# Kernel optimization log

Hardware: AMD Instinct MI355X
Metric: run time of the kernel (lower is better)

## Reference

```python
import jax, jax.numpy as jnp
import numpy as np

B, S, D_MODEL = 2, 2048, 512
KEY_DIM, VALUE_DIM, OUTPUT_DIM, NUM_HEADS = 256, 256, 512, 8


def setup_inputs() -> dict:
    key = jax.random.key(0)
    ks = jax.random.split(key, 12)
    s = 0.02
    return {
        "V": jax.random.normal(ks[0], (B, S, D_MODEL), jnp.float32),
        "Q": jax.random.normal(ks[1], (B, S, D_MODEL), jnp.float32),
        "K": jax.random.normal(ks[2], (B, S, D_MODEL), jnp.float32),
        "mask": jax.random.normal(ks[3], (B, 1, S, S), jnp.float32),
        "Wq": jax.random.normal(ks[4], (D_MODEL, KEY_DIM), jnp.float32) * s,
        "bq": jnp.zeros((KEY_DIM,), jnp.float32),
        "Wk": jax.random.normal(ks[5], (D_MODEL, KEY_DIM), jnp.float32) * s,
        "bk": jnp.zeros((KEY_DIM,), jnp.float32),
        "Wv": jax.random.normal(ks[6], (D_MODEL, VALUE_DIM), jnp.float32) * s,
        "bv": jnp.zeros((VALUE_DIM,), jnp.float32),
        "Wo": jax.random.normal(ks[7], (VALUE_DIM, OUTPUT_DIM), jnp.float32) * s,
        "bo": jnp.zeros((OUTPUT_DIM,), jnp.float32),
    }


def _split_heads(x, num_heads):
    # [B, S, H*d] -> [B, H, S, d]
    b, s, hd = x.shape
    return x.reshape(b, s, num_heads, hd // num_heads).transpose(0, 2, 1, 3)


def reference(V, Q, K, mask, Wq, bq, Wk, bk, Wv, bv, Wo, bo):
    denom = jnp.sqrt(jnp.float32(KEY_DIM))  # NOTE: full key_dim, as in source
    q = _split_heads(Q @ Wq + bq, NUM_HEADS)  # [B,H,S,dk]
    k = _split_heads(K @ Wk + bk, NUM_HEADS)
    scores = jnp.einsum("bhqd,bhkd->bhqk", q, k) / denom
    scores = scores + mask  # soft (additive) mask
    weights = jax.nn.softmax(scores, axis=-1)
    v = _split_heads(V @ Wv + bv, NUM_HEADS)  # [B,H,S,dv]
    ctx = jnp.einsum("bhqk,bhkd->bhqd", weights, v)  # [B,H,S,dv]
    b, h, s, d = ctx.shape
    ctx = ctx.transpose(0, 2, 1, 3).reshape(b, s, h * d)  # merge heads
    return ctx @ Wo + bo
```

## Files before the change

kernel.cpp:

```cpp
#include <hip/hip_runtime.h>

typedef __attribute__((ext_vector_type(8))) short bf16x8;
typedef __attribute__((ext_vector_type(4))) float f32x4;

#define B_  2
#define S_  2048
#define DM  512
#define KD  256
#define HD  32
#define NH  8

__device__ __forceinline__ float bf2f(ushort u) {
    return __uint_as_float(((uint)u) << 16);
}
__device__ __forceinline__ ushort f2bf(float f) {
    uint x = __float_as_uint(f);
    return (ushort)((x + 0x7fffu + ((x >> 16) & 1u)) >> 16);
}
#define MFMA __builtin_amdgcn_mfma_f32_16x16x32_bf16

__global__ void detect_dtype(const ushort* __restrict__ q, int* __restrict__ flag)
{
    int lane = threadIdx.x & 63;
    int cnt = 0;
    for (int i = lane; i < 256; i += 64) {
        int e = (q[i] >> 7) & 0xFF;
        if (e >= 100 && e <= 133) ++cnt;
    }
    #pragma unroll
    for (int off = 32; off; off >>= 1) cnt += __shfl_down(cnt, off, 64);
    if (lane == 0) *flag = (cnt >= 230) ? 1 : 0;
}

__global__ __launch_bounds__(256) void convert_x(
    const void* __restrict__ Q, const void* __restrict__ K, const void* __restrict__ V,
    const int* __restrict__ flag, ushort* __restrict__ Xb)
{
    int isbf = *flag;
    int y = blockIdx.y;
    int tid = blockIdx.x * 256 + threadIdx.x;
    const void* X = (y == 0) ? Q : (y == 1) ? K : V;
    ushort* dst = Xb + (size_t)y * (4096 * 512) + (size_t)tid * 8;
    if (isbf) {
        *(bf16x8*)dst = *((const bf16x8*)X + tid);
    } else {
        const float* s = (const float*)X + (size_t)tid * 8;
        bf16x8 v8;
        #pragma unroll
        for (int j = 0; j < 8; ++j) v8[j] = (short)f2bf(s[j]);
        *(bf16x8*)dst = v8;
    }
}

__global__ __launch_bounds__(256) void transpose_w(
    const void* __restrict__ Wq, const void* __restrict__ Wk, const void* __restrict__ Wv,
    const void* __restrict__ Wo,
    const void* __restrict__ bq, const void* __restrict__ bk,
    const void* __restrict__ bv, const void* __restrict__ bo,
    const int* __restrict__ flag,
    ushort* __restrict__ Wt, ushort* __restrict__ Wot, float* __restrict__ biasf)
{
    int isbf = *flag;
    int bid = blockIdx.x;
    if (bid >= 512) {
        for (int i = threadIdx.x; i < 1280; i += 256) {
            const void* bp; int off;
            if (i < 256)      { bp = bq; off = i; }
            else if (i < 512) { bp = bk; off = i - 256; }
            else if (i < 768) { bp = bv; off = i - 512; }
            else              { bp = bo; off = i - 768; }
            biasf[i] = isbf ? bf2f(((const ushort*)bp)[off]) : ((const float*)bp)[off];
        }
        return;
    }
    const void* W; int R, C; ushort* T;
    int m = bid >> 7, tix = bid & 127;
    if (m < 3) { W = (m == 0) ? Wq : (m == 1) ? Wk : Wv; R = 512; C = 256; T = Wt + m * 131072; }
    else       { W = Wo; R = 256; C = 512; T = Wot; }
    int tilesPerRow = C >> 5;
    int r0 = (tix / tilesPerRow) * 32, c0 = (tix % tilesPerRow) * 32;
    __shared__ float lds[32][33];
    int t = threadIdx.x;
    int rr = t >> 3, cc = (t & 7) * 4;
    if (isbf) {
        const ushort* Ws = (const ushort*)W;
        #pragma unroll
        for (int j = 0; j < 4; ++j) lds[rr][cc + j] = bf2f(Ws[(size_t)(r0 + rr) * C + c0 + cc + j]);
    } else {
        float4 v = *(const float4*)((const float*)W + (size_t)(r0 + rr) * C + c0 + cc);
        lds[rr][cc + 0] = v.x; lds[rr][cc + 1] = v.y; lds[rr][cc + 2] = v.z; lds[rr][cc + 3] = v.w;
    }
    __syncthreads();
    ushort4 o;
    o.x = f2bf(lds[cc + 0][rr]); o.y = f2bf(lds[cc + 1][rr]);
    o.z = f2bf(lds[cc + 2][rr]); o.w = f2bf(lds[cc + 3][rr]);
    *(ushort4*)(T + (size_t)(c0 + rr) * R + r0 + cc) = o;
}

__global__ __launch_bounds__(256) void qkv_gemm(
    const ushort* __restrict__ Xb, const ushort* __restrict__ Wt,
    const float* __restrict__ biasf,
    ushort* __restrict__ qh, ushort* __restrict__ kh, ushort* __restrict__ vh)
{
    int y = blockIdx.y;
    int wave = threadIdx.x >> 6, lane = threadIdx.x & 63;
    int l16 = lane & 15, quad = lane >> 4;
    int m0 = blockIdx.x * 32;
    int n0 = wave * 64;
    const ushort* X = Xb + (size_t)y * (4096 * 512);
    const ushort* W = Wt + (size_t)y * (256 * 512);
    f32x4 acc[2][4] = {};
    for (int ks = 0; ks < 512; ks += 32) {
        bf16x8 a[2], b[4];
        #pragma unroll
        for (int i = 0; i < 2; ++i)
            a[i] = *(const bf16x8*)(X + (size_t)(m0 + 16 * i + l16) * 512 + ks + quad * 8);
        #pragma unroll
        for (int j = 0; j < 4; ++j)
            b[j] = *(const bf16x8*)(W + (size_t)(n0 + 16 * j + l16) * 512 + ks + quad * 8);
        #pragma unroll
        for (int i = 0; i < 2; ++i)
            #pragma unroll
            for (int j = 0; j < 4; ++j)
                acc[i][j] = MFMA(a[i], b[j], acc[i][j], 0, 0, 0);
    }
    ushort* out = (y == 0) ? qh : (y == 1) ? kh : vh;
    #pragma unroll
    for (int i = 0; i < 2; ++i) {
        #pragma unroll
        for (int j = 0; j < 4; ++j) {
            int n = n0 + 16 * j + l16;
            float bs = biasf[y * 256 + n];
            int h = n >> 5, d = n & 31;
            #pragma unroll
            for (int r = 0; r < 4; ++r) {
                int rg = m0 + 16 * i + quad * 4 + r;
                int bb = rg >> 11, ss = rg & 2047;
                out[((((size_t)bb * NH + h) * S_ + ss) << 5) + d] = f2bf(acc[i][j][r] + bs);
            }
        }
    }
}

__global__ __launch_bounds__(256) void transpose_v(
    const ushort* __restrict__ vh, ushort* __restrict__ vT)
{
    __shared__ ushort lds[32][66];
    int bh = blockIdx.x >> 5;
    int s0 = (blockIdx.x & 31) * 64;
    int t = threadIdx.x;
    const ushort* src = vh + ((size_t)bh * S_ + s0) * HD;
    #pragma unroll
    for (int it = 0; it < 8; ++it) {
        int e = it * 256 + t;
        lds[e & 31][e >> 5] = src[e];
    }
    __syncthreads();
    ushort* dst = vT + (size_t)bh * HD * S_ + s0;
    #pragma unroll
    for (int it = 0; it < 8; ++it) {
        int e = it * 256 + t;
        dst[(size_t)(e >> 6) * S_ + (e & 63)] = lds[e >> 6][e & 63];
    }
}

__global__ __launch_bounds__(256) void attn(
    const ushort* __restrict__ qh, const ushort* __restrict__ kh,
    const ushort* __restrict__ vT, const void* __restrict__ maskp,
    const int* __restrict__ flag, float* __restrict__ pO, float* __restrict__ pl)
{
    __shared__ __align__(16) float  ldsM[4][16][68];
    __shared__ __align__(16) ushort ldsP[4][16][72];
    int isbf = *flag;
    int wave = threadIdx.x >> 6, lane = threadIdx.x & 63;
    int l16 = lane & 15, quad = lane >> 4;
    int wid = blockIdx.x * 4 + wave;
    int chunk = wid & 1, qt = (wid >> 1) & 127, bh = wid >> 8;
    int b = bh >> 3;
    int q0 = qt * 16;
    const ushort* qb = qh + (size_t)bh * S_ * HD;
    const ushort* kb = kh + (size_t)bh * S_ * HD;
    const ushort* vb = vT + (size_t)bh * HD * S_;
    const ushort* mbb = (const ushort*)maskp + (size_t)b * S_ * S_;
    const float*  mbf = (const float*)maskp  + (size_t)b * S_ * S_;

    bf16x8 aq = *(const bf16x8*)(qb + (size_t)(q0 + l16) * HD + quad * 8);
    f32x4 O0 = {0, 0, 0, 0}, O1 = {0, 0, 0, 0};
    const f32x4 zero = {0, 0, 0, 0};
    float lsum[4] = {0, 0, 0, 0};

    auto loadT = [&](int k0, float4* M, bf16x8* Kf, bf16x8* Vf) {
        if (isbf) {
            #pragma unroll
            for (int it = 0; it < 4; ++it) {
                ushort4 u = *(const ushort4*)(mbb + (size_t)(q0 + it * 4 + quad) * S_ + k0 + l16 * 4);
                float4 f; f.x = bf2f(u.x); f.y = bf2f(u.y); f.z = bf2f(u.z); f.w = bf2f(u.w);
                M[it] = f;
            }
        } else {
            #pragma unroll
            for (int it = 0; it < 4; ++it)
                M[it] = *(const float4*)(mbf + (size_t)(q0 + it * 4 + quad) * S_ + k0 + l16 * 4);
        }
        #pragma unroll
        for (int c = 0; c < 4; ++c)
            Kf[c] = *(const bf16x8*)(kb + (size_t)(k0 + c * 16 + l16) * HD + quad * 8);
        Vf[0] = *(const bf16x8*)(vb + (size_t)l16 * S_ + k0 + quad * 8);
        Vf[1] = *(const bf16x8*)(vb + (size_t)l16 * S_ + k0 + 32 + quad * 8);
        Vf[2] = *(const bf16x8*)(vb + (size_t)(16 + l16) * S_ + k0 + quad * 8);
        Vf[3] = *(const bf16x8*)(vb + (size_t)(16 + l16) * S_ + k0 + 32 + quad * 8);
    };

    auto tilestep = [&](float4* M, bf16x8* Kf, bf16x8* Vf,
                        int nextk0, float4* Mn, bf16x8* Kn, bf16x8* Vn) {
        #pragma unroll
        for (int it = 0; it < 4; ++it)
            *(float4*)&ldsM[wave][it * 4 + quad][l16 * 4] = M[it];
        if (nextk0 >= 0) loadT(nextk0, Mn, Kn, Vn);
        f32x4 Sc[4];
        #pragma unroll
        for (int c = 0; c < 4; ++c) Sc[c] = MFMA(aq, Kf[c], zero, 0, 0, 0);
        asm volatile("s_waitcnt lgkmcnt(0)" ::: "memory");
        #pragma unroll
        for (int c = 0; c < 4; ++c) {
            #pragma unroll
            for (int r = 0; r < 4; ++r) {
                float mv = ldsM[wave][quad * 4 + r][c * 16 + l16];
                float s = fminf(Sc[c][r] * 0.0625f + mv, 30.0f);
                float p = __expf(s);
                lsum[r] += p;
                ldsP[wave][quad * 4 + r][c * 16 + l16] = f2bf(p);
            }
        }
        asm volatile("s_waitcnt lgkmcnt(0)" ::: "memory");
        bf16x8 aP0 = *(const bf16x8*)&ldsP[wave][l16][quad * 8];
        bf16x8 aP1 = *(const bf16x8*)&ldsP[wave][l16][32 + quad * 8];
        O0 = MFMA(aP0, Vf[0], O0, 0, 0, 0);
        O0 = MFMA(aP1, Vf[1], O0, 0, 0, 0);
        O1 = MFMA(aP0, Vf[2], O1, 0, 0, 0);
        O1 = MFMA(aP1, Vf[3], O1, 0, 0, 0);
    };

    int kbase = chunk * 1024;
    float4 Ma[4], Mb2[4]; bf16x8 Ka[4], Kb2[4], Va[4], Vb2[4];
    loadT(kbase, Ma, Ka, Va);
    for (int t = 0; t < 16; t += 2) {
        tilestep(Ma, Ka, Va, kbase + (t + 1) * 64, Mb2, Kb2, Vb2);
        tilestep(Mb2, Kb2, Vb2, (t + 2 < 16) ? kbase + (t + 2) * 64 : -1, Ma, Ka, Va);
    }

    float* po = pO + (size_t)wid * 512;
    #pragma unroll
    for (int r = 0; r < 4; ++r) {
        int row = quad * 4 + r;
        po[row * 32 + l16]      = O0[r];
        po[row * 32 + 16 + l16] = O1[r];
        float sthis = lsum[r];
        #pragma unroll
        for (int off = 8; off; off >>= 1) sthis += __shfl_xor(sthis, off, 16);
        if (l16 == 0) pl[wid * 16 + row] = sthis;
    }
}

__global__ __launch_bounds__(256) void combine(
    const float* __restrict__ pO, const float* __restrict__ pl, ushort* __restrict__ ctx)
{
    int e = blockIdx.x * 256 + threadIdx.x;
    int d = e & 31;
    int row = (e >> 5) & 2047;
    int bh = e >> 16;
    int qt = row >> 4, r16 = row & 15;
    int wid0 = (bh << 8) | (qt << 1);
    float o = pO[(size_t)wid0 * 512 + r16 * 32 + d] + pO[(size_t)(wid0 + 1) * 512 + r16 * 32 + d];
    float l = pl[wid0 * 16 + r16] + pl[(wid0 + 1) * 16 + r16];
    int b = bh >> 3, h = bh & 7;
    ctx[((size_t)(b * S_ + row)) * KD + h * HD + d] = f2bf(o / l);
}

__global__ __launch_bounds__(256) void out_proj(
    const ushort* __restrict__ ctx, const ushort* __restrict__ Wot,
    const float* __restrict__ biasf, float* __restrict__ out)
{
    int wave = threadIdx.x >> 6, lane = threadIdx.x & 63;
    int l16 = lane & 15, quad = lane >> 4;
    int m0 = (blockIdx.x >> 1) * 32;
    int n0 = (blockIdx.x & 1) * 256 + wave * 64;
    f32x4 acc[2][4] = {};
    for (int ks = 0; ks < 256; ks += 32) {
        bf16x8 a[2], b[4];
        #pragma unroll
        for (int i = 0; i < 2; ++i)
            a[i] = *(const bf16x8*)(ctx + (size_t)(m0 + 16 * i + l16) * 256 + ks + quad * 8);
        #pragma unroll
        for (int j = 0; j < 4; ++j)
            b[j] = *(const bf16x8*)(Wot + (size_t)(n0 + 16 * j + l16) * 256 + ks + quad * 8);
        #pragma unroll
        for (int i = 0; i < 2; ++i)
            #pragma unroll
            for (int j = 0; j < 4; ++j)
                acc[i][j] = MFMA(a[i], b[j], acc[i][j], 0, 0, 0);
    }
    #pragma unroll
    for (int i = 0; i < 2; ++i) {
        #pragma unroll
        for (int j = 0; j < 4; ++j) {
            int n = n0 + 16 * j + l16;
            float bs = biasf[768 + n];
            #pragma unroll
            for (int r = 0; r < 4; ++r) {
                int rg = m0 + 16 * i + quad * 4 + r;
                out[(size_t)rg * DM + n] = acc[i][j][r] + bs;
            }
        }
    }
}

extern "C" void kernel_launch(void* const* d_in, const int* in_sizes, int n_in,
                              void* d_out, int out_size, void* d_ws, size_t ws_size,
                              hipStream_t stream)
{
    const void* V    = d_in[0];
    const void* Q    = d_in[1];
    const void* K    = d_in[2];
    const void* mask = d_in[3];
    const void* Wq = d_in[4];  const void* bq = d_in[5];
    const void* Wk = d_in[6];  const void* bk = d_in[7];
    const void* Wv = d_in[8];  const void* bv = d_in[9];
    const void* Wo = d_in[10]; const void* bo = d_in[11];
    float* out = (float*)d_out;

    char* ws = (char*)d_ws;
    int*    flagp = (int*)ws;
    float*  biasf = (float*)(ws + 128);
    ushort* qh  = (ushort*)(ws + 8192);
    ushort* kh  = qh  + 1048576;
    ushort* vh_ = kh  + 1048576;
    ushort* vT  = vh_ + 1048576;
    ushort* ctx = vT  + 1048576;
    ushort* Wt  = ctx + 1048576;
    ushort* Wot = Wt  + 393216;
    ushort* Xb  = Wot + 131072;
    float* pO = (float*)Xb;
    float* pl = pO + 4096 * 512;

    detect_dtype<<<1, 64, 0, stream>>>((const ushort*)Q, flagp);
    convert_x<<<dim3(1024, 3), 256, 0, stream>>>(Q, K, V, flagp, Xb);
    transpose_w<<<513, 256, 0, stream>>>(Wq, Wk, Wv, Wo, bq, bk, bv, bo, flagp, Wt, Wot, biasf);
    qkv_gemm<<<dim3(128, 3), 256, 0, stream>>>(Xb, Wt, biasf, qh, kh, vh_);
    transpose_v<<<512, 256, 0, stream>>>(vh_, vT);
    attn<<<1024, 256, 0, stream>>>(qh, kh, vT, mask, flagp, pO, pl);
    combine<<<4096, 256, 0, stream>>>(pO, pl, ctx);
    out_proj<<<256, 256, 0, stream>>>(ctx, Wot, biasf, out);
}
```

Baseline: 210.7 us.

## Fuse conversion, V transpose and combine into GEMMs; transpose attention MFMA layout

Removes the separate convert_x, transpose_v and combine kernels. The fp32-to-bf16 input conversion moves into the QKV GEMM's A loads, V is written already transposed from the GEMM epilogue, and the split-K combine plus normalization is folded into the output projection's A-operand load. The attention kernel computes S^T = K·Q so each lane holds mask values along contiguous keys, which drops the LDS staging of the mask and uses a single row sum per lane. This saves launches and intermediate global round-trips. In exchange the GEMMs re-convert and re-read inputs per tile, and the out_proj A loads become heavier.

Measured after the change: 230.6 us. 1.09x slower.

```diff
diff --git a/kernel.cpp b/kernel.cpp
--- a/kernel.cpp
+++ b/kernel.cpp
@@ -30,26 +30,6 @@
     #pragma unroll
     for (int off = 32; off; off >>= 1) cnt += __shfl_down(cnt, off, 64);
     if (lane == 0) *flag = (cnt >= 230) ? 1 : 0;
-}
-
-__global__ __launch_bounds__(256) void convert_x(
-    const void* __restrict__ Q, const void* __restrict__ K, const void* __restrict__ V,
-    const int* __restrict__ flag, ushort* __restrict__ Xb)
-{
-    int isbf = *flag;
-    int y = blockIdx.y;
-    int tid = blockIdx.x * 256 + threadIdx.x;
-    const void* X = (y == 0) ? Q : (y == 1) ? K : V;
-    ushort* dst = Xb + (size_t)y * (4096 * 512) + (size_t)tid * 8;
-    if (isbf) {
-        *(bf16x8*)dst = *((const bf16x8*)X + tid);
-    } else {
-        const float* s = (const float*)X + (size_t)tid * 8;
-        bf16x8 v8;
-        #pragma unroll
-        for (int j = 0; j < 8; ++j) v8[j] = (short)f2bf(s[j]);
-        *(bf16x8*)dst = v8;
-    }
 }
 
 __global__ __launch_bounds__(256) void transpose_w(
@@ -98,23 +78,37 @@
 }
 
 __global__ __launch_bounds__(256) void qkv_gemm(
-    const ushort* __restrict__ Xb, const ushort* __restrict__ Wt,
-    const float* __restrict__ biasf,
-    ushort* __restrict__ qh, ushort* __restrict__ kh, ushort* __restrict__ vh)
-{
+    const void* __restrict__ Q, const void* __restrict__ K, const void* __restrict__ V,
+    const ushort* __restrict__ Wt, const float* __restrict__ biasf,
+    const int* __restrict__ flag,
+    ushort* __restrict__ qh, ushort* __restrict__ kh, ushort* __restrict__ vT)
+{
+    int isbf = *flag;
     int y = blockIdx.y;
+    const void* X = (y == 0) ? Q : (y == 1) ? K : V;
     int wave = threadIdx.x >> 6, lane = threadIdx.x & 63;
     int l16 = lane & 15, quad = lane >> 4;
     int m0 = blockIdx.x * 32;
     int n0 = wave * 64;
-    const ushort* X = Xb + (size_t)y * (4096 * 512);
     const ushort* W = Wt + (size_t)y * (256 * 512);
     f32x4 acc[2][4] = {};
     for (int ks = 0; ks < 512; ks += 32) {
         bf16x8 a[2], b[4];
         #pragma unroll
-        for (int i = 0; i < 2; ++i)
-            a[i] = *(const bf16x8*)(X + (size_t)(m0 + 16 * i + l16) * 512 + ks + quad * 8);
+        for (int i = 0; i < 2; ++i) {
+            if (isbf) {
+                a[i] = *(const bf16x8*)((const ushort*)X + (size_t)(m0 + 16 * i + l16) * 512 + ks + quad * 8);
+            } else {
+                const float* p = (const float*)X + (size_t)(m0 + 16 * i + l16) * 512 + ks + quad * 8;
+                float4 f0 = *(const float4*)p, f1 = *(const float4*)(p + 4);
+                bf16x8 v8;
+                v8[0] = (short)f2bf(f0.x); v8[1] = (short)f2bf(f0.y);
+                v8[2] = (short)f2bf(f0.z); v8[3] = (short)f2bf(f0.w);
+                v8[4] = (short)f2bf(f1.x); v8[5] = (short)f2bf(f1.y);
+                v8[6] = (short)f2bf(f1.z); v8[7] = (short)f2bf(f1.w);
+                a[i] = v8;
+            }
+        }
         #pragma unroll
         for (int j = 0; j < 4; ++j)
             b[j] = *(const bf16x8*)(W + (size_t)(n0 + 16 * j + l16) * 512 + ks + quad * 8);
@@ -124,43 +118,39 @@
             for (int j = 0; j < 4; ++j)
                 acc[i][j] = MFMA(a[i], b[j], acc[i][j], 0, 0, 0);
     }
-    ushort* out = (y == 0) ? qh : (y == 1) ? kh : vh;
-    #pragma unroll
-    for (int i = 0; i < 2; ++i) {
-        #pragma unroll
-        for (int j = 0; j < 4; ++j) {
-            int n = n0 + 16 * j + l16;
-            float bs = biasf[y * 256 + n];
-            int h = n >> 5, d = n & 31;
-            #pragma unroll
-            for (int r = 0; r < 4; ++r) {
-                int rg = m0 + 16 * i + quad * 4 + r;
-                int bb = rg >> 11, ss = rg & 2047;
-                out[((((size_t)bb * NH + h) * S_ + ss) << 5) + d] = f2bf(acc[i][j][r] + bs);
-            }
-        }
-    }
-}
-
-__global__ __launch_bounds__(256) void transpose_v(
-    const ushort* __restrict__ vh, ushort* __restrict__ vT)
-{
-    __shared__ ushort lds[32][66];
-    int bh = blockIdx.x >> 5;
-    int s0 = (blockIdx.x & 31) * 64;
-    int t = threadIdx.x;
-    const ushort* src = vh + ((size_t)bh * S_ + s0) * HD;
-    #pragma unroll
-    for (int it = 0; it < 8; ++it) {
-        int e = it * 256 + t;
-        lds[e & 31][e >> 5] = src[e];
-    }
-    __syncthreads();
-    ushort* dst = vT + (size_t)bh * HD * S_ + s0;
-    #pragma unroll
-    for (int it = 0; it < 8; ++it) {
-        int e = it * 256 + t;
-        dst[(size_t)(e >> 6) * S_ + (e & 63)] = lds[e >> 6][e & 63];
+    if (y < 2) {
+        ushort* out = (y == 0) ? qh : kh;
+        #pragma unroll
+        for (int i = 0; i < 2; ++i) {
+            #pragma unroll
+            for (int j = 0; j < 4; ++j) {
+                int n = n0 + 16 * j + l16;
+                float bs = biasf[y * 256 + n];
+                int h = n >> 5, d = n & 31;
+                #pragma unroll
+                for (int r = 0; r < 4; ++r) {
+                    int rg = m0 + 16 * i + quad * 4 + r;
+                    int bb = rg >> 11, ss = rg & 2047;
+                    out[((((size_t)bb * NH + h) * S_ + ss) << 5) + d] = f2bf(acc[i][j][r] + bs);
+                }
+            }
+        }
+    } else {
+        #pragma unroll
+        for (int i = 0; i < 2; ++i) {
+            int rg0 = m0 + 16 * i + quad * 4;
+            int bb = rg0 >> 11, s0 = rg0 & 2047;
+            #pragma unroll
+            for (int j = 0; j < 4; ++j) {
+                int n = n0 + 16 * j + l16;
+                float bs = biasf[2 * 256 + n];
+                int h = n >> 5, d = n & 31;
+                ushort4 o;
+                o.x = f2bf(acc[i][j][0] + bs); o.y = f2bf(acc[i][j][1] + bs);
+                o.z = f2bf(acc[i][j][2] + bs); o.w = f2bf(acc[i][j][3] + bs);
+                *(ushort4*)(vT + (((size_t)(bb * NH + h) * HD + d) * S_) + s0) = o;
+            }
+        }
     }
 }
 
@@ -169,7 +159,6 @@
     const ushort* __restrict__ vT, const void* __restrict__ maskp,
     const int* __restrict__ flag, float* __restrict__ pO, float* __restrict__ pl)
 {
-    __shared__ __align__(16) float  ldsM[4][16][68];
     __shared__ __align__(16) ushort ldsP[4][16][72];
     int isbf = *flag;
     int wave = threadIdx.x >> 6, lane = threadIdx.x & 63;
@@ -181,105 +170,83 @@
     const ushort* qb = qh + (size_t)bh * S_ * HD;
     const ushort* kb = kh + (size_t)bh * S_ * HD;
     const ushort* vb = vT + (size_t)bh * HD * S_;
-    const ushort* mbb = (const ushort*)maskp + (size_t)b * S_ * S_;
-    const float*  mbf = (const float*)maskp  + (size_t)b * S_ * S_;
+    const ushort* mbb = (const ushort*)maskp + (size_t)b * S_ * S_ + (size_t)(q0 + l16) * S_;
+    const float*  mbf = (const float*)maskp  + (size_t)b * S_ * S_ + (size_t)(q0 + l16) * S_;
 
     bf16x8 aq = *(const bf16x8*)(qb + (size_t)(q0 + l16) * HD + quad * 8);
-    f32x4 O0 = {0, 0, 0, 0}, O1 = {0, 0, 0, 0};
+    f32x4 Od0 = {0, 0, 0, 0}, Od1 = {0, 0, 0, 0};
     const f32x4 zero = {0, 0, 0, 0};
-    float lsum[4] = {0, 0, 0, 0};
-
-    auto loadT = [&](int k0, float4* M, bf16x8* Kf, bf16x8* Vf) {
-        if (isbf) {
-            #pragma unroll
-            for (int it = 0; it < 4; ++it) {
-                ushort4 u = *(const ushort4*)(mbb + (size_t)(q0 + it * 4 + quad) * S_ + k0 + l16 * 4);
-                float4 f; f.x = bf2f(u.x); f.y = bf2f(u.y); f.z = bf2f(u.z); f.w = bf2f(u.w);
-                M[it] = f;
-            }
-        } else {
-            #pragma unroll
-            for (int it = 0; it < 4; ++it)
-                M[it] = *(const float4*)(mbf + (size_t)(q0 + it * 4 + quad) * S_ + k0 + l16 * 4);
-        }
+    float lsum = 0.f;
+
+    auto loadKM = [&](int k0, float4* M, bf16x8* Kf) {
         #pragma unroll
         for (int c = 0; c < 4; ++c)
             Kf[c] = *(const bf16x8*)(kb + (size_t)(k0 + c * 16 + l16) * HD + quad * 8);
-        Vf[0] = *(const bf16x8*)(vb + (size_t)l16 * S_ + k0 + quad * 8);
-        Vf[1] = *(const bf16x8*)(vb + (size_t)l16 * S_ + k0 + 32 + quad * 8);
-        Vf[2] = *(const bf16x8*)(vb + (size_t)(16 + l16) * S_ + k0 + quad * 8);
-        Vf[3] = *(const bf16x8*)(vb + (size_t)(16 + l16) * S_ + k0 + 32 + quad * 8);
+        if (isbf) {
+            #pragma unroll
+            for (int c = 0; c < 4; ++c) {
+                ushort4 u = *(const ushort4*)(mbb + k0 + c * 16 + quad * 4);
+                float4 f; f.x = bf2f(u.x); f.y = bf2f(u.y); f.z = bf2f(u.z); f.w = bf2f(u.w);
+                M[c] = f;
+            }
+        } else {
+            #pragma unroll
+            for (int c = 0; c < 4; ++c)
+                M[c] = *(const float4*)(mbf + k0 + c * 16 + quad * 4);
+        }
     };
 
-    auto tilestep = [&](float4* M, bf16x8* Kf, bf16x8* Vf,
-                        int nextk0, float4* Mn, bf16x8* Kn, bf16x8* Vn) {
-        #pragma unroll
-        for (int it = 0; it < 4; ++it)
-            *(float4*)&ldsM[wave][it * 4 + quad][l16 * 4] = M[it];
-        if (nextk0 >= 0) loadT(nextk0, Mn, Kn, Vn);
-        f32x4 Sc[4];
-        #pragma unroll
-        for (int c = 0; c < 4; ++c) Sc[c] = MFMA(aq, Kf[c], zero, 0, 0, 0);
+    auto tilestep = [&](int k0, float4* M, bf16x8* Kf,
+                        int nextk0, float4* Mn, bf16x8* Kn) {
+        bf16x8 Vf0 = *(const bf16x8*)(vb + (size_t)l16 * S_ + k0 + quad * 8);
+        bf16x8 Vf1 = *(const bf16x8*)(vb + (size_t)l16 * S_ + k0 + 32 + quad * 8);
+        bf16x8 Vf2 = *(const bf16x8*)(vb + (size_t)(16 + l16) * S_ + k0 + quad * 8);
+        bf16x8 Vf3 = *(const bf16x8*)(vb + (size_t)(16 + l16) * S_ + k0 + 32 + quad * 8);
+        f32x4 ST[4];
+        #pragma unroll
+        for (int c = 0; c < 4; ++c) ST[c] = MFMA(Kf[c], aq, zero, 0, 0, 0);
+        if (nextk0 >= 0) loadKM(nextk0, Mn, Kn);
+        #pragma unroll
+        for (int c = 0; c < 4; ++c) {
+            float p0 = __expf(fminf(ST[c][0] * 0.0625f + M[c].x, 30.0f));
+            float p1 = __expf(fminf(ST[c][1] * 0.0625f + M[c].y, 30.0f));
+            float p2 = __expf(fminf(ST[c][2] * 0.0625f + M[c].z, 30.0f));
+            float p3 = __expf(fminf(ST[c][3] * 0.0625f + M[c].w, 30.0f));
+            lsum += (p0 + p1) + (p2 + p3);
+            ushort4 pk;
+            pk.x = f2bf(p0); pk.y = f2bf(p1); pk.z = f2bf(p2); pk.w = f2bf(p3);
+            *(ushort4*)&ldsP[wave][l16][c * 16 + quad * 4] = pk;
+        }
         asm volatile("s_waitcnt lgkmcnt(0)" ::: "memory");
-        #pragma unroll
-        for (int c = 0; c < 4; ++c) {
-            #pragma unroll
-            for (int r = 0; r < 4; ++r) {
-                float mv = ldsM[wave][quad * 4 + r][c * 16 + l16];
-                float s = fminf(Sc[c][r] * 0.0625f + mv, 30.0f);
-                float p = __expf(s);
-                lsum[r] += p;
-                ldsP[wave][quad * 4 + r][c * 16 + l16] = f2bf(p);
-            }
-        }
-        asm volatile("s_waitcnt lgkmcnt(0)" ::: "memory");
-        bf16x8 aP0 = *(const bf16x8*)&ldsP[wave][l16][quad * 8];
-        bf16x8 aP1 = *(const bf16x8*)&ldsP[wave][l16][32 + quad * 8];
-        O0 = MFMA(aP0, Vf[0], O0, 0, 0, 0);
-        O0 = MFMA(aP1, Vf[1], O0, 0, 0, 0);
-        O1 = MFMA(aP0, Vf[2], O1, 0, 0, 0);
-        O1 = MFMA(aP1, Vf[3], O1, 0, 0, 0);
+        bf16x8 bP0 = *(const bf16x8*)&ldsP[wave][l16][quad * 8];
+        bf16x8 bP1 = *(const bf16x8*)&ldsP[wave][l16][32 + quad * 8];
+        Od0 = MFMA(Vf0, bP0, Od0, 0, 0, 0);
+        Od0 = MFMA(Vf1, bP1, Od0, 0, 0, 0);
+        Od1 = MFMA(Vf2, bP0, Od1, 0, 0, 0);
+        Od1 = MFMA(Vf3, bP1, Od1, 0, 0, 0);
     };
 
     int kbase = chunk * 1024;
-    float4 Ma[4], Mb2[4]; bf16x8 Ka[4], Kb2[4], Va[4], Vb2[4];
-    loadT(kbase, Ma, Ka, Va);
+    float4 Ma[4], Mb2[4]; bf16x8 Ka[4], Kb2[4];
+    loadKM(kbase, Ma, Ka);
     for (int t = 0; t < 16; t += 2) {
-        tilestep(Ma, Ka, Va, kbase + (t + 1) * 64, Mb2, Kb2, Vb2);
-        tilestep(Mb2, Kb2, Vb2, (t + 2 < 16) ? kbase + (t + 2) * 64 : -1, Ma, Ka, Va);
-    }
-
+        tilestep(kbase + t * 64, Ma, Ka, kbase + (t + 1) * 64, Mb2, Kb2);
+        tilestep(kbase + (t + 1) * 64, Mb2, Kb2,
+                 (t + 2 < 16) ? kbase + (t + 2) * 64 : -1, Ma, Ka);
+    }
+
+    lsum += __shfl_xor(lsum, 16, 64);
+    lsum += __shfl_xor(lsum, 32, 64);
     float* po = pO + (size_t)wid * 512;
-    #pragma unroll
-    for (int r = 0; r < 4; ++r) {
-        int row = quad * 4 + r;
-        po[row * 32 + l16]      = O0[r];
-        po[row * 32 + 16 + l16] = O1[r];
-        float sthis = lsum[r];
-        #pragma unroll
-        for (int off = 8; off; off >>= 1) sthis += __shfl_xor(sthis, off, 16);
-        if (l16 == 0) pl[wid * 16 + row] = sthis;
-    }
-}
-
-__global__ __launch_bounds__(256) void combine(
-    const float* __restrict__ pO, const float* __restrict__ pl, ushort* __restrict__ ctx)
-{
-    int e = blockIdx.x * 256 + threadIdx.x;
-    int d = e & 31;
-    int row = (e >> 5) & 2047;
-    int bh = e >> 16;
-    int qt = row >> 4, r16 = row & 15;
-    int wid0 = (bh << 8) | (qt << 1);
-    float o = pO[(size_t)wid0 * 512 + r16 * 32 + d] + pO[(size_t)(wid0 + 1) * 512 + r16 * 32 + d];
-    float l = pl[wid0 * 16 + r16] + pl[(wid0 + 1) * 16 + r16];
-    int b = bh >> 3, h = bh & 7;
-    ctx[((size_t)(b * S_ + row)) * KD + h * HD + d] = f2bf(o / l);
+    *(f32x4*)(po + l16 * 32 + quad * 4)      = Od0;
+    *(f32x4*)(po + l16 * 32 + 16 + quad * 4) = Od1;
+    if (quad == 0) pl[wid * 16 + l16] = lsum;
 }
 
 __global__ __launch_bounds__(256) void out_proj(
-    const ushort* __restrict__ ctx, const ushort* __restrict__ Wot,
-    const float* __restrict__ biasf, float* __restrict__ out)
+    const float* __restrict__ pO, const float* __restrict__ pl,
+    const ushort* __restrict__ Wot, const float* __restrict__ biasf,
+    float* __restrict__ out)
 {
     int wave = threadIdx.x >> 6, lane = threadIdx.x & 63;
     int l16 = lane & 15, quad = lane >> 4;
@@ -287,10 +254,25 @@
     int n0 = (blockIdx.x & 1) * 256 + wave * 64;
     f32x4 acc[2][4] = {};
     for (int ks = 0; ks < 256; ks += 32) {
+        int h = ks >> 5;
         bf16x8 a[2], b[4];
         #pragma unroll
-        for (int i = 0; i < 2; ++i)
-            a[i] = *(const bf16x8*)(ctx + (size_t)(m0 + 16 * i + l16) * 256 + ks + quad * 8);
+        for (int i = 0; i < 2; ++i) {
+            int row = m0 + 16 * i + l16;
+            int bb = row >> 11, s = row & 2047;
+            int qt = s >> 4, r16 = s & 15;
+            int wid0 = ((bb * NH + h) << 8) | (qt << 1);
+            const float* p0 = pO + (size_t)wid0 * 512 + r16 * 32 + quad * 8;
+            float4 x0 = *(const float4*)p0,      x1 = *(const float4*)(p0 + 4);
+            float4 y0 = *(const float4*)(p0 + 512), y1 = *(const float4*)(p0 + 516);
+            float il = 1.0f / (pl[wid0 * 16 + r16] + pl[(wid0 + 1) * 16 + r16]);
+            bf16x8 v8;
+            v8[0] = (short)f2bf((x0.x + y0.x) * il); v8[1] = (short)f2bf((x0.y + y0.y) * il);
+            v8[2] = (short)f2bf((x0.z + y0.z) * il); v8[3] = (short)f2bf((x0.w + y0.w) * il);
+            v8[4] = (short)f2bf((x1.x + y1.x) * il); v8[5] = (short)f2bf((x1.y + y1.y) * il);
+            v8[6] = (short)f2bf((x1.z + y1.z) * il); v8[7] = (short)f2bf((x1.w + y1.w) * il);
+            a[i] = v8;
+        }
         #pragma unroll
         for (int j = 0; j < 4; ++j)
             b[j] = *(const bf16x8*)(Wot + (size_t)(n0 + 16 * j + l16) * 256 + ks + quad * 8);
@@ -332,23 +314,17 @@
     char* ws = (char*)d_ws;
     int*    flagp = (int*)ws;
     float*  biasf = (float*)(ws + 128);
-    ushort* qh  = (ushort*)(ws + 8192);
+    ushort* Wt  = (ushort*)(ws + 8192);
+    ushort* Wot = Wt  + 393216;
+    ushort* qh  = Wot + 131072;
     ushort* kh  = qh  + 1048576;
-    ushort* vh_ = kh  + 1048576;
-    ushort* vT  = vh_ + 1048576;
-    ushort* ctx = vT  + 1048576;
-    ushort* Wt  = ctx + 1048576;
-    ushort* Wot = Wt  + 393216;
-    ushort* Xb  = Wot + 131072;
-    float* pO = (float*)Xb;
-    float* pl = pO + 4096 * 512;
+    ushort* vT  = kh  + 1048576;
+    float*  pO  = (float*)(vT + 1048576);
+    float*  pl  = pO + 4096 * 512;
 
     detect_dtype<<<1, 64, 0, stream>>>((const ushort*)Q, flagp);
-    convert_x<<<dim3(1024, 3), 256, 0, stream>>>(Q, K, V, flagp, Xb);
     transpose_w<<<513, 256, 0, stream>>>(Wq, Wk, Wv, Wo, bq, bk, bv, bo, flagp, Wt, Wot, biasf);
-    qkv_gemm<<<dim3(128, 3), 256, 0, stream>>>(Xb, Wt, biasf, qh, kh, vh_);
-    transpose_v<<<512, 256, 0, stream>>>(vh_, vT);
+    qkv_gemm<<<dim3(128, 3), 256, 0, stream>>>(Q, K, V, Wt, biasf, flagp, qh, kh, vT);
     attn<<<1024, 256, 0, stream>>>(qh, kh, vT, mask, flagp, pO, pl);
-    combine<<<4096, 256, 0, stream>>>(pO, pl, ctx);
-    out_proj<<<256, 256, 0, stream>>>(ctx, Wot, biasf, out);
-}
+    out_proj<<<256, 256, 0, stream>>>(pO, pl, Wot, biasf, out);
+}
```
